# Optimization experiments

Hardware: AMD Instinct MI355X
Metric: run time of the kernel (lower is better)

## Reference

```python
import jax, jax.numpy as jnp
import numpy as np

# Config (matches init_kwargs)
IN_CH = 128
HID = 128
HEADS = 1
B, H, W = 8, 192, 192


def setup_inputs() -> dict:
    key = jax.random.key(0)
    ks = jax.random.split(key, 10)
    s = 0.05
    x = jax.random.normal(ks[0], (B, IN_CH, H, W), dtype=jnp.float32)
    # 1x1 conv weights stored as (out, in); bias (out,)
    Wq = jax.random.normal(ks[1], (HID, IN_CH), dtype=jnp.float32) * s
    bq = jax.random.normal(ks[2], (HID,), dtype=jnp.float32) * s
    Wk = jax.random.normal(ks[3], (HID, IN_CH), dtype=jnp.float32) * s
    bk = jax.random.normal(ks[4], (HID,), dtype=jnp.float32) * s
    Wv = jax.random.normal(ks[5], (HID, IN_CH), dtype=jnp.float32) * s
    bv = jax.random.normal(ks[6], (HID,), dtype=jnp.float32) * s
    Wo = jax.random.normal(ks[7], (IN_CH, HID), dtype=jnp.float32) * s
    bo = jax.random.normal(ks[8], (IN_CH,), dtype=jnp.float32) * s
    gamma = jax.random.normal(ks[9], (1,), dtype=jnp.float32) * 0.5
    return {"x": x, "Wq": Wq, "bq": bq, "Wk": Wk, "bk": bk,
            "Wv": Wv, "bv": bv, "Wo": Wo, "bo": bo, "gamma": gamma}


def _conv1x1(x, Wt, b):
    # x: (B, Cin, H, W); Wt: (Cout, Cin) -> (B, Cout, H, W)
    return jnp.einsum('oc,bchw->bohw', Wt, x) + b[None, :, None, None]


def reference(x, Wq, bq, Wk, bk, Wv, bv, Wo, bo, gamma):
    b, c, h, w = x.shape
    n = h * w
    d = HID // HEADS
    # q/k/v: (B, hidden, H, W) -> view(B, d, heads, N) -> (B*heads, d, N)
    def proj(Wt, bias):
        y = _conv1x1(x, Wt, bias).reshape(b, d, HEADS, n)
        return jnp.transpose(y, (0, 2, 1, 3)).reshape(b * HEADS, d, n)
    q = proj(Wq, bq)
    k = proj(Wk, bk)
    v = proj(Wv, bv)
    # NOTE: energy is d x d (channel attention), contracted over N. No scale.
    energy = jnp.einsum('bdn,ben->bde', q, k)        # (B*heads, d, d)
    attention = jax.nn.softmax(energy, axis=-1)
    attn_out = jnp.einsum('bde,ben->bdn', attention, v)  # (B*heads, d, N)
    attn_out = attn_out.reshape(b, HEADS, d, n)
    attn_out = jnp.transpose(attn_out, (0, 2, 1, 3)).reshape(b, HID, h, w)
    attn_out = _conv1x1(attn_out, Wo, bo)
    return gamma * attn_out + x
```

## Files before the change

### kernel.cpp

```cpp
#include <hip/hip_runtime.h>
#include <cstdint>
#include <cstddef>

#define NB  8
#define NC  128
#define NHW 36864

#define GOFF  0
#define SOFF  131072
#define TOFF  132096
#define ROFF  133120
#define CVOFF 264192
#define MHOFF 265216
#define MLOFF 330752

typedef __attribute__((ext_vector_type(8))) short short8;
typedef __attribute__((ext_vector_type(4))) float f32x4;

static __device__ __forceinline__ f32x4 zero4(){ f32x4 v = {0.f,0.f,0.f,0.f}; return v; }

static __device__ __forceinline__ short bfbits(float f){
    union { __bf16 b; short s; } u; u.b = (__bf16)f; return u.s;
}
static __device__ __forceinline__ void cv2(float f, short& hb, short& lb){
    union { __bf16 b; short s; } u;
    u.b = (__bf16)f; hb = u.s;
    float hf = (float)u.b;
    u.b = (__bf16)(f - hf); lb = u.s;
}
static __device__ __forceinline__ float cv8(f32x4 v0, f32x4 v1, short8& h, short8& l){
    float ss = 0.f;
#pragma unroll
    for (int j=0;j<4;j++){
        short hb, lb;
        cv2(v0[j], hb, lb); h[j]   = hb; l[j]   = lb;
        cv2(v1[j], hb, lb); h[4+j] = hb; l[4+j] = lb;
        ss += v0[j] + v1[j];
    }
    return ss;
}

__global__ __launch_bounds__(256) void k_zero(float* __restrict__ p){
    const int i = (blockIdx.x*256 + threadIdx.x)*4;
    *(f32x4*)(p + i) = zero4();
}

#define GNT 36
#define GLDH 5120

__global__ __launch_bounds__(512) void k_gram(const float* __restrict__ x,
                                              float* __restrict__ G,
                                              float* __restrict__ svec){
    __shared__ short Ls[2][2][GLDH];
    const int b     = blockIdx.y;
    const int chunk = blockIdx.x;
    const int tid   = threadIdx.x;
    const int wid   = tid >> 6, lane = tid & 63;
    const int l16   = lane & 15, lgi = lane >> 4;
    const int sr    = tid >> 2;
    const int sc    = (tid & 3) * 8;

    const float* xs = x + (size_t)b*NC*NHW + (size_t)sr*NHW + chunk*1152 + sc;

    float srow = 0.f;
    f32x4 acc[8];
#pragma unroll
    for (int g=0;g<8;g++) acc[g] = zero4();

    const int ra = (wid*16 + l16)*40 + lgi*8;

    {
        f32x4 v0 = *(const f32x4*)(xs);
        f32x4 v1 = *(const f32x4*)(xs+4);
        short8 h0,l0;
        srow += cv8(v0,v1,h0,l0);
        *(short8*)&Ls[0][0][sr*40 + sc] = h0;
        *(short8*)&Ls[0][1][sr*40 + sc] = l0;
    }
    __syncthreads();

    for (int t=0; t<GNT-1; ++t){
        const float* p = xs + (t+1)*32;
        f32x4 v0 = *(const f32x4*)(p);
        f32x4 v1 = *(const f32x4*)(p+4);
        __builtin_amdgcn_sched_barrier(0);

        {
            const short* Lh = Ls[t&1][0];
            const short* Ll = Ls[t&1][1];
            short8 hA = *(const short8*)(Lh + ra);
            short8 lA = *(const short8*)(Ll + ra);
#pragma unroll
            for (int g=0; g<8; g++){
                const int rb = (g*16 + l16)*40 + lgi*8;
                short8 hg  = *(const short8*)(Lh + rb);
                short8 lg2 = *(const short8*)(Ll + rb);
                acc[g] = __builtin_amdgcn_mfma_f32_16x16x32_bf16(hA, hg,  acc[g], 0,0,0);
                acc[g] = __builtin_amdgcn_mfma_f32_16x16x32_bf16(hA, lg2, acc[g], 0,0,0);
                acc[g] = __builtin_amdgcn_mfma_f32_16x16x32_bf16(lA, hg,  acc[g], 0,0,0);
            }
        }

        {
            short8 h0,l0;
            srow += cv8(v0,v1,h0,l0);
            *(short8*)&Ls[(t+1)&1][0][sr*40 + sc] = h0;
            *(short8*)&Ls[(t+1)&1][1][sr*40 + sc] = l0;
        }
        __syncthreads();
    }

    {
        const short* Lh = Ls[(GNT-1)&1][0];
        const short* Ll = Ls[(GNT-1)&1][1];
        short8 hA = *(const short8*)(Lh + ra);
        short8 lA = *(const short8*)(Ll + ra);
#pragma unroll
        for (int g=0; g<8; g++){
            const int rb = (g*16 + l16)*40 + lgi*8;
            short8 hg  = *(const short8*)(Lh + rb);
            short8 lg2 = *(const short8*)(Ll + rb);
            acc[g] = __builtin_amdgcn_mfma_f32_16x16x32_bf16(hA, hg,  acc[g], 0,0,0);
            acc[g] = __builtin_amdgcn_mfma_f32_16x16x32_bf16(hA, lg2, acc[g], 0,0,0);
            acc[g] = __builtin_amdgcn_mfma_f32_16x16x32_bf16(lA, hg,  acc[g], 0,0,0);
        }
    }

    float* Gb = G + (size_t)b*NC*NC;
#pragma unroll
    for (int g=0;g<8;g++){
#pragma unroll
        for (int r=0;r<4;r++){
            atomicAdd(&Gb[(size_t)(wid*16 + lgi*4 + r)*NC + g*16 + l16], acc[g][r]);
        }
    }
    srow += __shfl_xor(srow, 1);
    srow += __shfl_xor(srow, 2);
    if ((tid & 3) == 0) atomicAdd(&svec[b*NC + sr], srow);
}

__global__ __launch_bounds__(256) void k_energyav(const float* __restrict__ G,
        const float* __restrict__ svec,
        const float* __restrict__ Wq, const float* __restrict__ bq,
        const float* __restrict__ Wk, const float* __restrict__ bk,
        const float* __restrict__ bv, const float* __restrict__ Wv,
        float* __restrict__ R, float* __restrict__ tvec){
    const int b  = blockIdx.y;
    const int d0 = blockIdx.x * 16;
    const int tid = threadIdx.x;
    const int d  = tid & 15;
    const int ec = tid >> 4;

    __shared__ float Ps[16][128];
    __shared__ float Es[16][128];
    __shared__ float red[16][16];
    __shared__ float rowmax[16];
    __shared__ float rowsum[16];
    __shared__ float qs[16];

    const float* Wqrow = Wq + (size_t)(d0 + d)*NC;
    const float* sb = svec + b*NC;
#pragma unroll
    for (int i=0;i<8;i++){
        const int c = ec*8 + i;
        const float* Grow = G + ((size_t)b*NC + c)*NC;
        float a = 0.f;
        for (int c4=0;c4<32;c4++){
            f32x4 g4 = *(const f32x4*)(Grow + c4*4);
            f32x4 w4 = *(const f32x4*)(Wqrow + c4*4);
            a += g4[0]*w4[0] + g4[1]*w4[1] + g4[2]*w4[2] + g4[3]*w4[3];
        }
        Ps[d][c] = a;
    }
    if (ec == 0){
        float a = 0.f;
        for (int c4=0;c4<32;c4++){
            f32x4 w4 = *(const f32x4*)(Wqrow + c4*4);
            f32x4 s4 = *(const f32x4*)(sb + c4*4);
            a += w4[0]*s4[0] + w4[1]*s4[1] + w4[2]*s4[2] + w4[3]*s4[3];
        }
        qs[d] = a;
    }
    __syncthreads();
    const float bqd = bq[d0+d];
#pragma unroll
    for (int i=0;i<8;i++){
        const int e = ec*8 + i;
        const float* Wkrow = Wk + (size_t)e*NC;
        float ea = 0.f, ks = 0.f;
        for (int c4=0;c4<32;c4++){
            f32x4 w4 = *(const f32x4*)(Wkrow + c4*4);
            f32x4 p4 = *(const f32x4*)(&Ps[d][c4*4]);
            f32x4 s4 = *(const f32x4*)(sb + c4*4);
            ea += w4[0]*p4[0]+w4[1]*p4[1]+w4[2]*p4[2]+w4[3]*p4[3];
            ks += w4[0]*s4[0]+w4[1]*s4[1]+w4[2]*s4[2]+w4[3]*s4[3];
        }
        const float bke = bk[e];
        Es[d][e] = ea + bke*qs[d] + bqd*ks + (float)NHW*bqd*bke;
    }
    float m8 = -3.4e38f;
#pragma unroll
    for (int i=0;i<8;i++) m8 = fmaxf(m8, Es[d][ec*8+i]);
    red[d][ec] = m8;
    __syncthreads();
    if (tid < 16){
        float m = red[tid][0];
        for (int j=1;j<16;j++) m = fmaxf(m, red[tid][j]);
        rowmax[tid] = m;
    }
    __syncthreads();
    const float rm = rowmax[d];
    float s8 = 0.f;
#pragma unroll
    for (int i=0;i<8;i++){
        float ex = expf(Es[d][ec*8+i] - rm);
        Es[d][ec*8+i] = ex;
        s8 += ex;
    }
    red[d][ec] = s8;
    __syncthreads();
    if (tid < 16){
        float sm = 0.f;
        for (int j=0;j<16;j++) sm += red[tid][j];
        rowsum[tid] = sm;
    }
    __syncthreads();
    const float inv = 1.f / rowsum[d];
    float ta = 0.f;
#pragma unroll
    for (int i=0;i<8;i++){
        const int e = ec*8 + i;
        float av = Es[d][e] * inv;
        Es[d][e] = av;
        ta += av * bv[e];
    }
    red[d][ec] = ta;
    __syncthreads();
    if (tid < 16){
        float sm = 0.f;
        for (int j=0;j<16;j++) sm += red[tid][j];
        tvec[b*NC + d0 + tid] = sm;
    }
    const int c0 = ec*8;
    float racc[8];
#pragma unroll
    for (int i=0;i<8;i++) racc[i]=0.f;
    for (int e=0;e<NC;e++){
        const float av = Es[d][e];
        const float* wv = Wv + (size_t)e*NC + c0;
        f32x4 w0 = *(const f32x4*)wv;
        f32x4 w1 = *(const f32x4*)(wv+4);
        racc[0]+=av*w0[0]; racc[1]+=av*w0[1]; racc[2]+=av*w0[2]; racc[3]+=av*w0[3];
        racc[4]+=av*w1[0]; racc[5]+=av*w1[1]; racc[6]+=av*w1[2]; racc[7]+=av*w1[3];
    }
    float* Rrow = R + ((size_t)b*NC + d0 + d)*NC + c0;
#pragma unroll
    for (int i=0;i<8;i++) Rrow[i] = racc[i];
}

__global__ __launch_bounds__(256) void k_om(const float* __restrict__ R,
        const float* __restrict__ Wo, const float* __restrict__ bo,
        const float* __restrict__ tvec, const float* __restrict__ gamma,
        short* __restrict__ Mh_, short* __restrict__ Ml_, float* __restrict__ cvg){
    const int b = blockIdx.y, o0 = blockIdx.x*16;
    const int tid = threadIdx.x, o = tid&15, cc = tid>>4;
    const int c0 = cc*8;
    const float* Worow = Wo + (size_t)(o0+o)*NC;
    const float* tb = tvec + b*NC;
    float a[8];
#pragma unroll
    for (int i=0;i<8;i++) a[i]=0.f;
    float cv = 0.f;
    for (int dd=0; dd<NC; dd++){
        const float wv = Worow[dd];
        const float* r = R + ((size_t)b*NC + dd)*NC + c0;
        f32x4 r0 = *(const f32x4*)r;
        f32x4 r1 = *(const f32x4*)(r+4);
        a[0]+=wv*r0[0]; a[1]+=wv*r0[1]; a[2]+=wv*r0[2]; a[3]+=wv*r0[3];
        a[4]+=wv*r1[0]; a[5]+=wv*r1[1]; a[6]+=wv*r1[2]; a[7]+=wv*r1[3];
        cv += wv*tb[dd];
    }
    const float gm = gamma[0];
    const int c   = o0 + o;
    const int cg  = c >> 4;
    const int kst = cc >> 2, lgv = cc & 3;
    const size_t idx = ((((size_t)b*8 + cg)*4 + kst)*64 + (lgv*16 + (c & 15)))*8;
    short8 hh, ll;
#pragma unroll
    for (int i=0;i<8;i++){
        float val = gm*a[i] + ((c0 + i) == c ? 1.f : 0.f);
        short hb, lb; cv2(val, hb, lb);
        hh[i]=hb; ll[i]=lb;
    }
    *(short8*)(Mh_ + idx) = hh;
    *(short8*)(Ml_ + idx) = ll;
    if (cc == 0) cvg[b*NC + c] = gm*(cv + bo[c]);
}

__global__ __launch_bounds__(256, 4) void k_final(const float* __restrict__ x,
        const short* __restrict__ Mh_, const short* __restrict__ Ml_,
        const float* __restrict__ cvg, float* __restrict__ out){
    __shared__ short Xt[NC*128];
    const int b   = blockIdx.y;
    const int n0  = blockIdx.x * 128;
    const int tid = threadIdx.x;
    const int wid = tid >> 6, lane = tid & 63;
    const int l16 = lane & 15, lgi = lane >> 4;

    const int nr = tid & 31, mb8 = tid >> 5;
    const float* xs = x + (size_t)b*NC*NHW + n0 + nr*4;
#pragma unroll
    for (int rep=0; rep<2; rep++){
        const int m0 = rep*64 + mb8*8;
        const float* xm = xs + (size_t)m0*NHW;
        f32x4 v0 = *(const f32x4*)(xm);
        f32x4 v1 = *(const f32x4*)(xm + (size_t)1*NHW);
        f32x4 v2 = *(const f32x4*)(xm + (size_t)2*NHW);
        f32x4 v3 = *(const f32x4*)(xm + (size_t)3*NHW);
        f32x4 v4 = *(const f32x4*)(xm + (size_t)4*NHW);
        f32x4 v5 = *(const f32x4*)(xm + (size_t)5*NHW);
        f32x4 v6 = *(const f32x4*)(xm + (size_t)6*NHW);
        f32x4 v7 = *(const f32x4*)(xm + (size_t)7*NHW);
#pragma unroll
        for (int r=0;r<4;r++){
            short8 w;
            w[0]=bfbits(v0[r]); w[1]=bfbits(v1[r]); w[2]=bfbits(v2[r]); w[3]=bfbits(v3[r]);
            w[4]=bfbits(v4[r]); w[5]=bfbits(v5[r]); w[6]=bfbits(v6[r]); w[7]=bfbits(v7[r]);
            const int n = nr*4 + r;
            const int slot = (rep*8 + mb8) ^ ((n>>2)&15) ^ ((n&3)<<2);
            *(short8*)(&Xt[n*128 + slot*8]) = w;
        }
    }
    __syncthreads();

    f32x4 acc[2][8];
#pragma unroll
    for (int t=0;t<2;t++)
#pragma unroll
      for (int g=0;g<8;g++) acc[t][g]=zero4();

    const short* Mh = Mh_ + (size_t)b*16384;
    const short* Ml = Ml_ + (size_t)b*16384;

#pragma unroll
    for (int ks=0; ks<4; ks++){
        const int nA0 = wid*32 + l16;
        const int nA1 = nA0 + 16;
        const int sl  = ks*4 + lgi;
        const int s0  = sl ^ ((nA0>>2)&15) ^ ((nA0&3)<<2);
        const int s1  = sl ^ ((nA1>>2)&15) ^ ((nA1&3)<<2);
        short8 a0 = *(const short8*)(&Xt[nA0*128 + s0*8]);
        short8 a1 = *(const short8*)(&Xt[nA1*128 + s1*8]);
#pragma unroll
        for (int cg=0; cg<8; cg++){
            const size_t bi = (((size_t)cg*4 + ks)*64 + lane)*8;
            short8 bh = *(const short8*)(Mh + bi);
            short8 bl = *(const short8*)(Ml + bi);
            acc[0][cg] = __builtin_amdgcn_mfma_f32_16x16x32_bf16(a0, bh, acc[0][cg], 0,0,0);
            acc[0][cg] = __builtin_amdgcn_mfma_f32_16x16x32_bf16(a0, bl, acc[0][cg], 0,0,0);
            acc[1][cg] = __builtin_amdgcn_mfma_f32_16x16x32_bf16(a1, bh, acc[1][cg], 0,0,0);
            acc[1][cg] = __builtin_amdgcn_mfma_f32_16x16x32_bf16(a1, bl, acc[1][cg], 0,0,0);
        }
    }

    const float* cb = cvg + b*NC;
#pragma unroll
    for (int cg=0;cg<8;cg++){
        const int c = cg*16 + l16;
        const float ccv = cb[c];
        float* orow = &out[((size_t)b*NC + c)*NHW + n0 + wid*32 + lgi*4];
#pragma unroll
        for (int t=0;t<2;t++){
            f32x4 o = acc[t][cg];
            o[0]+=ccv; o[1]+=ccv; o[2]+=ccv; o[3]+=ccv;
            *(f32x4*)(orow + t*16) = o;
        }
    }
}

extern "C" void kernel_launch(void* const* d_in, const int* in_sizes, int n_in,
                              void* d_out, int out_size, void* d_ws, size_t ws_size,
                              hipStream_t stream){
    const float* x     = (const float*)d_in[0];
    const float* Wq    = (const float*)d_in[1];
    const float* bq    = (const float*)d_in[2];
    const float* Wk    = (const float*)d_in[3];
    const float* bk    = (const float*)d_in[4];
    const float* Wv    = (const float*)d_in[5];
    const float* bv    = (const float*)d_in[6];
    const float* Wo    = (const float*)d_in[7];
    const float* bo    = (const float*)d_in[8];
    const float* gamma = (const float*)d_in[9];
    float* out = (float*)d_out;

    float* w  = (float*)d_ws;
    float* G  = w + GOFF;
    float* S  = w + SOFF;
    float* T  = w + TOFF;
    float* R  = w + ROFF;
    float* CV = w + CVOFF;
    short* Mh = (short*)(w + MHOFF);
    short* Ml = (short*)(w + MLOFF);

    k_zero    <<<dim3(129),     256, 0, stream>>>(G);

    k_gram    <<<dim3(32,  NB), 512, 0, stream>>>(x, G, S);
    k_energyav<<<dim3(8,   NB), 256, 0, stream>>>(G, S, Wq, bq, Wk, bk, bv, Wv, R, T);
    k_om      <<<dim3(8,   NB), 256, 0, stream>>>(R, Wo, bo, T, gamma, Mh, Ml, CV);
    k_final   <<<dim3(288, NB), 256, 0, stream>>>(x, Mh, Ml, CV, out);
}
```

Baseline: 195.7 us.

## Drop hi/lo bf16 split in final GEMM, add exact fp32 residual, double gram grid

The final output GEMM now uses a single bf16 copy of gamma*M instead of a hi/lo split with the identity folded in. This halves the MFMA count and the weight loads in k_final. The residual x is added back in fp32 by re-reading x in the epilogue, so the identity term stays exact. The cost is an extra global read of x and lower precision in the attention term. The gram kernel grid also doubles, with half-size chunks per block, to raise parallelism.

```diff
diff --git a/kernel.cpp b/kernel.cpp
--- a/kernel.cpp
+++ b/kernel.cpp
@@ -11,8 +11,7 @@
 #define TOFF  132096
 #define ROFF  133120
 #define CVOFF 264192
-#define MHOFF 265216
-#define MLOFF 330752
+#define MBOFF 265216
 
 typedef __attribute__((ext_vector_type(8))) short short8;
 typedef __attribute__((ext_vector_type(4))) float f32x4;
@@ -45,7 +44,7 @@
     *(f32x4*)(p + i) = zero4();
 }
 
-#define GNT 36
+#define GNT 18
 #define GLDH 5120
 
 __global__ __launch_bounds__(512) void k_gram(const float* __restrict__ x,
@@ -60,7 +59,7 @@
     const int sr    = tid >> 2;
     const int sc    = (tid & 3) * 8;
 
-    const float* xs = x + (size_t)b*NC*NHW + (size_t)sr*NHW + chunk*1152 + sc;
+    const float* xs = x + (size_t)b*NC*NHW + (size_t)sr*NHW + chunk*576 + sc;
 
     float srow = 0.f;
     f32x4 acc[8];
@@ -261,7 +260,7 @@
 __global__ __launch_bounds__(256) void k_om(const float* __restrict__ R,
         const float* __restrict__ Wo, const float* __restrict__ bo,
         const float* __restrict__ tvec, const float* __restrict__ gamma,
-        short* __restrict__ Mh_, short* __restrict__ Ml_, float* __restrict__ cvg){
+        short* __restrict__ Mb_, float* __restrict__ cvg){
     const int b = blockIdx.y, o0 = blockIdx.x*16;
     const int tid = threadIdx.x, o = tid&15, cc = tid>>4;
     const int c0 = cc*8;
@@ -285,21 +284,16 @@
     const int cg  = c >> 4;
     const int kst = cc >> 2, lgv = cc & 3;
     const size_t idx = ((((size_t)b*8 + cg)*4 + kst)*64 + (lgv*16 + (c & 15)))*8;
-    short8 hh, ll;
-#pragma unroll
-    for (int i=0;i<8;i++){
-        float val = gm*a[i] + ((c0 + i) == c ? 1.f : 0.f);
-        short hb, lb; cv2(val, hb, lb);
-        hh[i]=hb; ll[i]=lb;
-    }
-    *(short8*)(Mh_ + idx) = hh;
-    *(short8*)(Ml_ + idx) = ll;
+    short8 hh;
+#pragma unroll
+    for (int i=0;i<8;i++) hh[i] = bfbits(gm*a[i]);
+    *(short8*)(Mb_ + idx) = hh;
     if (cc == 0) cvg[b*NC + c] = gm*(cv + bo[c]);
 }
 
 __global__ __launch_bounds__(256, 4) void k_final(const float* __restrict__ x,
-        const short* __restrict__ Mh_, const short* __restrict__ Ml_,
-        const float* __restrict__ cvg, float* __restrict__ out){
+        const short* __restrict__ Mb_, const float* __restrict__ cvg,
+        float* __restrict__ out){
     __shared__ short Xt[NC*128];
     const int b   = blockIdx.y;
     const int n0  = blockIdx.x * 128;
@@ -339,8 +333,7 @@
 #pragma unroll
       for (int g=0;g<8;g++) acc[t][g]=zero4();
 
-    const short* Mh = Mh_ + (size_t)b*16384;
-    const short* Ml = Ml_ + (size_t)b*16384;
+    const short* Mb = Mb_ + (size_t)b*16384;
 
 #pragma unroll
     for (int ks=0; ks<4; ks++){
@@ -353,13 +346,9 @@
         short8 a1 = *(const short8*)(&Xt[nA1*128 + s1*8]);
 #pragma unroll
         for (int cg=0; cg<8; cg++){
-            const size_t bi = (((size_t)cg*4 + ks)*64 + lane)*8;
-            short8 bh = *(const short8*)(Mh + bi);
-            short8 bl = *(const short8*)(Ml + bi);
+            short8 bh = *(const short8*)(Mb + (((size_t)cg*4 + ks)*64 + lane)*8);
             acc[0][cg] = __builtin_amdgcn_mfma_f32_16x16x32_bf16(a0, bh, acc[0][cg], 0,0,0);
-            acc[0][cg] = __builtin_amdgcn_mfma_f32_16x16x32_bf16(a0, bl, acc[0][cg], 0,0,0);
             acc[1][cg] = __builtin_amdgcn_mfma_f32_16x16x32_bf16(a1, bh, acc[1][cg], 0,0,0);
-            acc[1][cg] = __builtin_amdgcn_mfma_f32_16x16x32_bf16(a1, bl, acc[1][cg], 0,0,0);
         }
     }
 
@@ -368,11 +357,14 @@
     for (int cg=0;cg<8;cg++){
         const int c = cg*16 + l16;
         const float ccv = cb[c];
-        float* orow = &out[((size_t)b*NC + c)*NHW + n0 + wid*32 + lgi*4];
+        const size_t rowoff = ((size_t)b*NC + c)*NHW + n0 + wid*32 + lgi*4;
+        const float* xrow = &x[rowoff];
+        float* orow = &out[rowoff];
 #pragma unroll
         for (int t=0;t<2;t++){
+            f32x4 xv = *(const f32x4*)(xrow + t*16);
             f32x4 o = acc[t][cg];
-            o[0]+=ccv; o[1]+=ccv; o[2]+=ccv; o[3]+=ccv;
+            o[0]+=ccv+xv[0]; o[1]+=ccv+xv[1]; o[2]+=ccv+xv[2]; o[3]+=ccv+xv[3];
             *(f32x4*)(orow + t*16) = o;
         }
     }
@@ -399,13 +391,12 @@
     float* T  = w + TOFF;
     float* R  = w + ROFF;
     float* CV = w + CVOFF;
-    short* Mh = (short*)(w + MHOFF);
-    short* Ml = (short*)(w + MLOFF);
+    short* Mb = (short*)(w + MBOFF);
 
     k_zero    <<<dim3(129),     256, 0, stream>>>(G);
 
-    k_gram    <<<dim3(32,  NB), 512, 0, stream>>>(x, G, S);
+    k_gram    <<<dim3(64,  NB), 512, 0, stream>>>(x, G, S);
     k_energyav<<<dim3(8,   NB), 256, 0, stream>>>(G, S, Wq, bq, Wk, bk, bv, Wv, R, T);
-    k_om      <<<dim3(8,   NB), 256, 0, stream>>>(R, Wo, bo, T, gamma, Mh, Ml, CV);
-    k_final   <<<dim3(288, NB), 256, 0, stream>>>(x, Mh, Ml, CV, out);
-}
+    k_om      <<<dim3(8,   NB), 256, 0, stream>>>(R, Wo, bo, T, gamma, Mb, CV);
+    k_final   <<<dim3(288, NB), 256, 0, stream>>>(x, Mb, CV, out);
+}
```

New measurement: 206.3 us. 5.4% more time.
